# Kernel tuning notes

Hardware: AMD Instinct MI355X
Metric: run time of the kernel (lower is better)

## Reference

```python
import jax, jax.numpy as jnp
import numpy as np

V, E, U = 50257, 256, 256
B, T = 32, 512


def setup_inputs() -> dict:
    key = jax.random.key(0)
    ks = jax.random.split(key, 8)
    s = 0.02  # small init keeps relu-LSTM numerically stable over 512 steps
    return {
        "tokens": jax.random.randint(ks[0], (B, T), 0, V, dtype=jnp.int32),
        "emb": jax.random.normal(ks[1], (V, E), jnp.float32) * s,
        "Wk_f": jax.random.normal(ks[2], (E, 4 * U), jnp.float32) * s,
        "Wr_f": jax.random.normal(ks[3], (U, 4 * U), jnp.float32) * s,
        "b_f": jnp.zeros((4 * U,), jnp.float32),
        "Wk_b": jax.random.normal(ks[4], (E, 4 * U), jnp.float32) * s,
        "Wr_b": jax.random.normal(ks[5], (U, 4 * U), jnp.float32) * s,
        "b_b": jnp.zeros((4 * U,), jnp.float32),
    }


def _lstm_relu(xw, mask, Wr):
    """xw: [T,B,4U] precomputed x@Wk+b; mask: [T,B,1] bool; Wr: [U,4U].
    Keras LSTM with activation='relu', recurrent_activation='sigmoid',
    gate order i,f,g,o. Masked steps carry state & output."""
    u = Wr.shape[0]
    b = xw.shape[1]
    h0 = jnp.zeros((b, u), xw.dtype)
    c0 = jnp.zeros((b, u), xw.dtype)

    def step(carry, inp):
        h, c = carry
        z_x, m = inp
        z = z_x + h @ Wr  # [B,4U]
        i, f, g, o = jnp.split(z, 4, axis=-1)
        i = jax.nn.sigmoid(i)
        f = jax.nn.sigmoid(f)
        g = jax.nn.relu(g)
        o = jax.nn.sigmoid(o)
        c_new = f * c + i * g
        h_new = o * jax.nn.relu(c_new)
        h2 = jnp.where(m, h_new, h)
        c2 = jnp.where(m, c_new, c)
        return (h2, c2), h2

    (hT, cT), ys = jax.lax.scan(step, (h0, c0), (xw, mask))
    return ys, hT, cT  # ys: [T,B,U]


def reference(tokens, emb, Wk_f, Wr_f, b_f, Wk_b, Wr_b, b_b):
    x = emb[tokens]                    # [B,T,E]
    mask = (tokens != 0)[..., None]    # [B,T,1] mask_zero=True
    # forward direction
    xw_f = (x @ Wk_f + b_f).transpose(1, 0, 2)   # [T,B,4U]
    m_f = mask.transpose(1, 0, 2)                # [T,B,1]
    ys_f, hf, cf = _lstm_relu(xw_f, m_f, Wr_f)
    # backward direction: reversed sequence, then re-reverse outputs
    xw_b = (x @ Wk_b + b_b)[:, ::-1].transpose(1, 0, 2)
    m_b = mask[:, ::-1].transpose(1, 0, 2)
    ys_b, hb, cb = _lstm_relu(xw_b, m_b, Wr_b)
    ys_b = ys_b[::-1]
    encoder_outputs = jnp.concatenate([ys_f, ys_b], axis=-1).transpose(1, 0, 2)  # [B,T,2U]
    # NOTE: original module concatenates f_state_h with b_state_c (bug kept faithfully)
    encoder_state_h = jnp.concatenate([hf, cb], axis=-1)  # [B,2U]
    encoder_state_c = jnp.concatenate([cf, cb], axis=-1)  # [B,2U]
    return encoder_outputs, encoder_state_h, encoder_state_c
```

## Files before the change

kernel.cpp:

```cpp
#include <hip/hip_runtime.h>
#include <hip/hip_bf16.h>

#define TT 512
#define BB 32
#define EE 256
#define UU 256
#define NG 1024

typedef unsigned int u32;
typedef unsigned long long u64;
typedef unsigned short u16;
typedef __attribute__((ext_vector_type(8))) short short8;
typedef __attribute__((ext_vector_type(4))) float f32x4;

__device__ __forceinline__ float bf2f(u16 u) { return __uint_as_float(((u32)u) << 16); }
__device__ __forceinline__ u16 f2bf(float f) {
    u32 x = __float_as_uint(f);
    u32 r = (x + 0x7fffu + ((x >> 16) & 1u)) >> 16;
    return (u16)r;
}

__launch_bounds__(256)
__global__ void xw_gemm(const int* __restrict__ tokens,
                        const float* __restrict__ emb,
                        const float* __restrict__ Wk_f, const float* __restrict__ b_f,
                        const float* __restrict__ Wk_b, const float* __restrict__ b_b,
                        u16* __restrict__ xw)
{
    const int dir = blockIdx.z;
    const float* Wk   = dir ? Wk_b : Wk_f;
    const float* bias = dir ? b_b  : b_f;
    const int bn = blockIdx.x;
    const int bm = blockIdx.y;
    const int tid = threadIdx.x;

    __shared__ __align__(16) float At[32][68];
    __shared__ __align__(16) float Bs[32][132];

    float acc[8][4];
#pragma unroll
    for (int i = 0; i < 8; i++)
#pragma unroll
        for (int j = 0; j < 4; j++) acc[i][j] = 0.f;

    const int tx = tid & 31;
    const int ty = tid >> 5;
    const int c0 = tx * 4;
    const int r0 = ty * 8;

    const int lr = tid >> 3;
    const int lk = (tid & 7) * 4;

    for (int k0 = 0; k0 < EE; k0 += 32) {
#pragma unroll
        for (int p = 0; p < 2; p++) {
            int r = lr + p * 32;
            int row = bm * 64 + r;
            int tok = tokens[row];
            const float4 v = *reinterpret_cast<const float4*>(&emb[(size_t)tok * EE + k0 + lk]);
            At[lk + 0][r] = v.x; At[lk + 1][r] = v.y; At[lk + 2][r] = v.z; At[lk + 3][r] = v.w;
        }
        {
            int ck = (tid & 31) * 4;
            int kk = tid >> 5;
#pragma unroll
            for (int p = 0; p < 4; p++) {
                int k = kk + p * 8;
                const float4 v = *reinterpret_cast<const float4*>(&Wk[(size_t)(k0 + k) * NG + bn * 128 + ck]);
                *reinterpret_cast<float4*>(&Bs[k][ck]) = v;
            }
        }
        __syncthreads();
#pragma unroll 8
        for (int k = 0; k < 32; k++) {
            float4 a0 = *reinterpret_cast<const float4*>(&At[k][r0]);
            float4 a1 = *reinterpret_cast<const float4*>(&At[k][r0 + 4]);
            float4 b0 = *reinterpret_cast<const float4*>(&Bs[k][c0]);
            float a[8] = {a0.x, a0.y, a0.z, a0.w, a1.x, a1.y, a1.z, a1.w};
            float b[4] = {b0.x, b0.y, b0.z, b0.w};
#pragma unroll
            for (int i = 0; i < 8; i++)
#pragma unroll
                for (int j = 0; j < 4; j++)
                    acc[i][j] = fmaf(a[i], b[j], acc[i][j]);
        }
        __syncthreads();
    }

    float4 bv = *reinterpret_cast<const float4*>(&bias[bn * 128 + c0]);
    float bias4[4] = {bv.x, bv.y, bv.z, bv.w};
    const int cbase = bn * 128 + c0;
    const int gate  = cbase >> 8;
    const int unitv = cbase & 255;
    const int ugx   = unitv >> 5;
    const int wcol  = gate * 32 + (unitv & 31);
#pragma unroll
    for (int i = 0; i < 8; i++) {
        int row = bm * 64 + r0 + i;
        int b = row >> 9;
        int t = row & 511;
        int t2 = dir ? (TT - 1 - t) : t;
        size_t base = ((((size_t)(dir * TT + t2)) * 8 + ugx) * BB + b) * 128 + wcol;
        ushort4 st;
        st.x = f2bf(acc[i][0] + bias4[0]);
        st.y = f2bf(acc[i][1] + bias4[1]);
        st.z = f2bf(acc[i][2] + bias4[2]);
        st.w = f2bf(acc[i][3] + bias4[3]);
        *reinterpret_cast<ushort4*>(&xw[base]) = st;
    }
}

__device__ __forceinline__ u64 ld_agent(const u64* p) {
    return __hip_atomic_load(p, __ATOMIC_RELAXED, __HIP_MEMORY_SCOPE_AGENT);
}

__launch_bounds__(256, 1)
__global__ void lstm_rec(const int* __restrict__ tokens,
                         const u16* __restrict__ xw,
                         const float* __restrict__ Wr_f,
                         const float* __restrict__ Wr_b,
                         u64* __restrict__ hgq,
                         float* __restrict__ out)
{
    const int wg  = blockIdx.x;
    const int dir = wg >> 3;
    const int ug  = wg & 7;
    const int unit0 = ug * 32;
    const int tid = threadIdx.x;
    const int wv  = tid >> 6;
    const int l   = tid & 63;

    __shared__ __align__(16) u32   HsW[32 * 128];
    __shared__ __align__(16) float Zs[2][BB][132];

    const float* Wr = dir ? Wr_b : Wr_f;
    short8 bfrag[8][2];
    {
        const int col = wv * UU + unit0 + (l & 15);
#pragma unroll
        for (int kt = 0; kt < 8; kt++) {
#pragma unroll
            for (int nt = 0; nt < 2; nt++) {
                int k0 = kt * 32 + (l >> 4) * 8;
                short8 v;
#pragma unroll
                for (int jj = 0; jj < 8; jj++)
                    v[jj] = (short)f2bf(Wr[(size_t)(k0 + jj) * NG + col + nt * 16]);
                bfrag[kt][nt] = v;
            }
        }
    }

    const int cb = tid >> 3;
    const int cj = tid & 7;
    float c_st[4] = {0.f, 0.f, 0.f, 0.f};
    float h_st[4] = {0.f, 0.f, 0.f, 0.f};

    const u16* xwD = xw + (size_t)dir * TT * 8 * BB * 128;
    u64 pxw[4];
    int ptok;
    {
        const u16* p = xwD + (((size_t)0 * 8 + ug) * BB + cb) * 128 + cj * 4;
#pragma unroll
        for (int g = 0; g < 4; g++)
            pxw[g] = *reinterpret_cast<const u64*>(p + g * 32);
        ptok = tokens[cb * TT + (dir ? (TT - 1) : 0)];
    }

    float* outs_h = out + (size_t)BB * TT * 512;
    float* outs_c = outs_h + (size_t)BB * 512;

    for (int s = 0; s < TT; s++) {
        const int p = s & 1;
        f32x4 acc[2][2];
#pragma unroll
        for (int mt = 0; mt < 2; mt++)
#pragma unroll
            for (int nt = 0; nt < 2; nt++) acc[mt][nt] = (f32x4){0.f, 0.f, 0.f, 0.f};

        if (s > 0) {
            const u64* hb = hgq + (size_t)(p * 2 + dir) * 4096 + wv * 1024 + l;
            const u64 tp = (u64)(u32)s | ((u64)(u32)s << 32);
            u64 ql[16];
#pragma unroll
            for (int j = 0; j < 16; j++) ql[j] = ld_agent(hb + j * 64);
            while (true) {
                u64 bad = 0;
#pragma unroll
                for (int j = 0; j < 16; j++) bad |= ql[j] ^ tp;
                if (__all((bad & 0x0000FFFF0000FFFFull) == 0ull)) break;
                __builtin_amdgcn_s_sleep(1);
#pragma unroll
                for (int j = 0; j < 16; j++) ql[j] = ld_agent(hb + j * 64);
            }
#pragma unroll
            for (int j = 0; j < 16; j++) {
                u32 w32 = (((u32)(ql[j] >> 16)) & 0xFFFFu) | (((u32)(ql[j] >> 48)) << 16);
                int ugs = wv * 2 + (j >> 3);
                int b   = (j * 4 + (l >> 4)) & 31;
                int pos = l & 15;
                int g   = ugs * 4 + (pos >> 2);
                HsW[b * 128 + ((g ^ (b & 7)) << 2) + (pos & 3)] = w32;
            }
            __syncthreads();

#pragma unroll
            for (int kt = 0; kt < 8; kt++) {
#pragma unroll
                for (int mt = 0; mt < 2; mt++) {
                    int b = mt * 16 + (l & 15);
                    int g = kt * 4 + (l >> 4);
                    short8 af = *reinterpret_cast<const short8*>(
                        &HsW[b * 128 + ((g ^ (b & 7)) << 2)]);
                    acc[mt][0] = __builtin_amdgcn_mfma_f32_16x16x32_bf16(af, bfrag[kt][0], acc[mt][0], 0, 0, 0);
                    acc[mt][1] = __builtin_amdgcn_mfma_f32_16x16x32_bf16(af, bfrag[kt][1], acc[mt][1], 0, 0, 0);
                }
            }
        }

#pragma unroll
        for (int mt = 0; mt < 2; mt++)
#pragma unroll
            for (int nt = 0; nt < 2; nt++)
#pragma unroll
                for (int r = 0; r < 4; r++)
                    Zs[p][mt * 16 + (l >> 4) * 4 + r][wv * 32 + nt * 16 + (l & 15)] = acc[mt][nt][r];
        __syncthreads();

        float h2[4], c2[4];
        {
            const bool m = (ptok != 0);
#pragma unroll
            for (int q = 0; q < 4; q++) {
                float zi = Zs[p][cb][0 * 32 + cj * 4 + q] + bf2f((u16)(pxw[0] >> (16 * q)));
                float zf = Zs[p][cb][1 * 32 + cj * 4 + q] + bf2f((u16)(pxw[1] >> (16 * q)));
                float zg = Zs[p][cb][2 * 32 + cj * 4 + q] + bf2f((u16)(pxw[2] >> (16 * q)));
                float zo = Zs[p][cb][3 * 32 + cj * 4 + q] + bf2f((u16)(pxw[3] >> (16 * q)));
                float ii = 1.f / (1.f + __expf(-zi));
                float ff = 1.f / (1.f + __expf(-zf));
                float gg = fmaxf(zg, 0.f);
                float oo = 1.f / (1.f + __expf(-zo));
                float cn = ff * c_st[q] + ii * gg;
                float hn = oo * fmaxf(cn, 0.f);
                h2[q] = m ? hn : h_st[q];
                c2[q] = m ? cn : c_st[q];
                h_st[q] = h2[q];
                c_st[q] = c2[q];
            }
        }

        {
            const u32 tagn = (u32)(s + 1);
            u32 t0 = ((u32)f2bf(h2[0]) << 16) | tagn;
            u32 t1 = ((u32)f2bf(h2[1]) << 16) | tagn;
            u32 t2 = ((u32)f2bf(h2[2]) << 16) | tagn;
            u32 t3 = ((u32)f2bf(h2[3]) << 16) | tagn;
            u64 lo = (u64)t0 | ((u64)t1 << 32);
            u64 hi = (u64)t2 | ((u64)t3 << 32);
            u64* hd = hgq + (size_t)(((s + 1) & 1) * 2 + dir) * 4096 + (ug * 32 + cb) * 16 + cj * 2;
            __hip_atomic_store(hd + 0, lo, __ATOMIC_RELAXED, __HIP_MEMORY_SCOPE_AGENT);
            __hip_atomic_store(hd + 1, hi, __ATOMIC_RELAXED, __HIP_MEMORY_SCOPE_AGENT);
        }

        const int tv = dir ? (TT - 1 - s) : s;
        *reinterpret_cast<float4*>(&out[((size_t)cb * TT + tv) * 512 + dir * UU + unit0 + cj * 4]) =
            make_float4(h2[0], h2[1], h2[2], h2[3]);
        if (s == TT - 1) {
            if (dir == 0) {
                *reinterpret_cast<float4*>(&outs_h[cb * 512 + unit0 + cj * 4]) = make_float4(h2[0], h2[1], h2[2], h2[3]);
                *reinterpret_cast<float4*>(&outs_c[cb * 512 + unit0 + cj * 4]) = make_float4(c2[0], c2[1], c2[2], c2[3]);
            } else {
                *reinterpret_cast<float4*>(&outs_h[cb * 512 + UU + unit0 + cj * 4]) = make_float4(c2[0], c2[1], c2[2], c2[3]);
                *reinterpret_cast<float4*>(&outs_c[cb * 512 + UU + unit0 + cj * 4]) = make_float4(c2[0], c2[1], c2[2], c2[3]);
            }
        }
        if (s + 1 < TT) {
            const u16* px = xwD + (((size_t)(s + 1) * 8 + ug) * BB + cb) * 128 + cj * 4;
#pragma unroll
            for (int g = 0; g < 4; g++)
                pxw[g] = *reinterpret_cast<const u64*>(px + g * 32);
            ptok = tokens[cb * TT + (dir ? (TT - 2 - s) : (s + 1))];
        }
    }
}

extern "C" void kernel_launch(void* const* d_in, const int* in_sizes, int n_in,
                              void* d_out, int out_size, void* d_ws, size_t ws_size,
                              hipStream_t stream) {
    const int*   tokens = (const int*)d_in[0];
    const float* emb    = (const float*)d_in[1];
    const float* Wk_f   = (const float*)d_in[2];
    const float* Wr_f   = (const float*)d_in[3];
    const float* b_f    = (const float*)d_in[4];
    const float* Wk_b   = (const float*)d_in[5];
    const float* Wr_b   = (const float*)d_in[6];
    const float* b_b    = (const float*)d_in[7];
    float* out = (float*)d_out;

    char* ws = (char*)d_ws;
    u16* xw  = (u16*)ws;
    u64* hgq = (u64*)(ws + 67108864);

    hipMemsetAsync(hgq, 0, 262144, stream);
    dim3 g1(8, 256, 2);
    xw_gemm<<<g1, 256, 0, stream>>>(tokens, emb, Wk_f, b_f, Wk_b, b_b, xw);
    lstm_rec<<<16, 256, 0, stream>>>(tokens, xw, Wr_f, Wr_b, hgq, out);
}
```

Before: 1.683 ms.

## Co-locate recurrent workgroups on one XCD and poll h-state through L2

Launches 128 workgroups and uses an atomic election on the hardware XCC ID to keep 16 active workgroups on a single XCD (or split across two). The other workgroups exit. Polling of the exchanged hidden state then uses sc0 global loads that are served from that XCD's shared L2, which should cut per-step cross-die synchronisation latency. If polling keeps failing it falls back to agent-scope polling and periodically re-stores its own data. Per-launch epoch-hashed tags replace the memset of the exchange buffer. The change also prefetches the next step's xw earlier and uses nontemporal output stores. It adds risks: 16-bit tags can collide with stale data, the control words live in the tail of the output buffer, and correctness depends on timeouts and restores.

```diff
diff --git a/kernel.cpp b/kernel.cpp
--- a/kernel.cpp
+++ b/kernel.cpp
@@ -12,6 +12,9 @@
 typedef unsigned short u16;
 typedef __attribute__((ext_vector_type(8))) short short8;
 typedef __attribute__((ext_vector_type(4))) float f32x4;
+typedef __attribute__((ext_vector_type(4))) u32 u32x4;
+
+#define TAGMASK 0x0000FFFF0000FFFFull
 
 __device__ __forceinline__ float bf2f(u16 u) { return __uint_as_float(((u32)u) << 16); }
 __device__ __forceinline__ u16 f2bf(float f) {
@@ -114,24 +117,98 @@
     return __hip_atomic_load(p, __ATOMIC_RELAXED, __HIP_MEMORY_SCOPE_AGENT);
 }
 
+__device__ __forceinline__ void poll16_l2(u64 b0, u32 voff, u64* q) {
+    asm volatile(
+        "global_load_dwordx2 %[q0], %[vo], %[b0] sc0\n\t"
+        "global_load_dwordx2 %[q1], %[vo], %[b0] offset:512 sc0\n\t"
+        "global_load_dwordx2 %[q2], %[vo], %[b0] offset:1024 sc0\n\t"
+        "global_load_dwordx2 %[q3], %[vo], %[b0] offset:1536 sc0\n\t"
+        "global_load_dwordx2 %[q4], %[vo], %[b0] offset:2048 sc0\n\t"
+        "global_load_dwordx2 %[q5], %[vo], %[b0] offset:2560 sc0\n\t"
+        "global_load_dwordx2 %[q6], %[vo], %[b0] offset:3072 sc0\n\t"
+        "global_load_dwordx2 %[q7], %[vo], %[b0] offset:3584 sc0\n\t"
+        "global_load_dwordx2 %[q8], %[vo], %[b1] sc0\n\t"
+        "global_load_dwordx2 %[q9], %[vo], %[b1] offset:512 sc0\n\t"
+        "global_load_dwordx2 %[q10], %[vo], %[b1] offset:1024 sc0\n\t"
+        "global_load_dwordx2 %[q11], %[vo], %[b1] offset:1536 sc0\n\t"
+        "global_load_dwordx2 %[q12], %[vo], %[b1] offset:2048 sc0\n\t"
+        "global_load_dwordx2 %[q13], %[vo], %[b1] offset:2560 sc0\n\t"
+        "global_load_dwordx2 %[q14], %[vo], %[b1] offset:3072 sc0\n\t"
+        "global_load_dwordx2 %[q15], %[vo], %[b1] offset:3584 sc0\n\t"
+        "s_waitcnt vmcnt(0)"
+        : [q0]"=&v"(q[0]), [q1]"=&v"(q[1]), [q2]"=&v"(q[2]), [q3]"=&v"(q[3]),
+          [q4]"=&v"(q[4]), [q5]"=&v"(q[5]), [q6]"=&v"(q[6]), [q7]"=&v"(q[7]),
+          [q8]"=&v"(q[8]), [q9]"=&v"(q[9]), [q10]"=&v"(q[10]), [q11]"=&v"(q[11]),
+          [q12]"=&v"(q[12]), [q13]"=&v"(q[13]), [q14]"=&v"(q[14]), [q15]"=&v"(q[15])
+        : [vo]"v"(voff), [b0]"s"(b0), [b1]"s"(b0 + 4096ull)
+        : "memory");
+}
+
+__device__ __forceinline__ void dual_store(u64* hd, u64 lo, u64 hi) {
+    u32x4 v = (u32x4){(u32)lo, (u32)(lo >> 32), (u32)hi, (u32)(hi >> 32)};
+    asm volatile("global_store_dwordx4 %[a], %[d], off sc0"
+                 :: [a]"v"(hd), [d]"v"(v) : "memory");
+    __hip_atomic_store(hd + 0, lo, __ATOMIC_RELAXED, __HIP_MEMORY_SCOPE_AGENT);
+    __hip_atomic_store(hd + 1, hi, __ATOMIC_RELAXED, __HIP_MEMORY_SCOPE_AGENT);
+}
+
 __launch_bounds__(256, 1)
 __global__ void lstm_rec(const int* __restrict__ tokens,
                          const u16* __restrict__ xw,
                          const float* __restrict__ Wr_f,
                          const float* __restrict__ Wr_b,
                          u64* __restrict__ hgq,
+                         int* __restrict__ ctl,
                          float* __restrict__ out)
 {
-    const int wg  = blockIdx.x;
-    const int dir = wg >> 3;
-    const int ug  = wg & 7;
+    const int tid = threadIdx.x;
+
+    __shared__ int s_role, s_epoch;
+    __shared__ __align__(16) u32   HsW[32 * 128];
+    __shared__ __align__(16) float Zs[2][BB][132];
+
+    if (tid == 0) {
+        u32 xcc;
+        asm volatile("s_getreg_b32 %0, hwreg(HW_REG_XCC_ID)" : "=s"(xcc));
+        xcc &= 7u;
+        u32* cnt = (u32*)(ctl + 4);
+        u32 slot = atomicAdd(&cnt[xcc], 1u);
+        if (slot == 7u) {
+            if (atomicCAS(&ctl[0], -1, (int)xcc) == -1) {
+                u64 rt = __builtin_amdgcn_s_memrealtime();
+                int ep = (int)((((u32)rt ^ (u32)(rt >> 32)) & 0x7FFFFFFEu) | 1u);
+                atomicExch(&ctl[2], ep);
+            } else {
+                atomicCAS(&ctl[1], -1, (int)xcc);
+            }
+        } else if (slot == 15u) {
+            atomicCAS(&ctl[1], -1, (int)xcc);
+        }
+        int w0, w1, ep;
+        for (;;) {
+            w0 = __hip_atomic_load(&ctl[0], __ATOMIC_RELAXED, __HIP_MEMORY_SCOPE_AGENT);
+            w1 = __hip_atomic_load(&ctl[1], __ATOMIC_RELAXED, __HIP_MEMORY_SCOPE_AGENT);
+            ep = __hip_atomic_load(&ctl[2], __ATOMIC_RELAXED, __HIP_MEMORY_SCOPE_AGENT);
+            if (w0 >= 0 && w1 >= 0 && ep != -1) break;
+            __builtin_amdgcn_s_sleep(8);
+        }
+        int role = -1;
+        if ((int)xcc == w0 && slot < 8u) role = (int)slot;
+        else if (w1 == w0 && (int)xcc == w0 && slot >= 8u && slot < 16u) role = (int)slot;
+        else if (w1 != w0 && (int)xcc == w1 && slot < 8u) role = 8 + (int)slot;
+        s_role = role;
+        s_epoch = ep;
+    }
+    __syncthreads();
+    const int role = s_role;
+    const u32 tagbase = (u32)s_epoch * 2654435761u;
+    if (role < 0) return;
+
+    const int dir = role >> 3;
+    const int ug  = role & 7;
     const int unit0 = ug * 32;
-    const int tid = threadIdx.x;
     const int wv  = tid >> 6;
     const int l   = tid & 63;
-
-    __shared__ __align__(16) u32   HsW[32 * 128];
-    __shared__ __align__(16) float Zs[2][BB][132];
 
     const float* Wr = dir ? Wr_b : Wr_f;
     short8 bfrag[8][2];
@@ -155,6 +232,18 @@
     const int cj = tid & 7;
     float c_st[4] = {0.f, 0.f, 0.f, 0.f};
     float h_st[4] = {0.f, 0.f, 0.f, 0.f};
+
+    u64* const hdP[2] = {
+        hgq + (size_t)(0 * 2 + dir) * 4096 + (ug * 32 + cb) * 16 + cj * 2,
+        hgq + (size_t)(1 * 2 + dir) * 4096 + (ug * 32 + cb) * 16 + cj * 2
+    };
+    u64 myLo[2] = {0ull, 0ull}, myHi[2] = {0ull, 0ull};
+
+    auto restoreMine = [&](int s_) {
+        const int cpar = s_ & 1;
+        dual_store(hdP[cpar], myLo[cpar], myHi[cpar]);
+        if (s_ >= 2) dual_store(hdP[cpar ^ 1], myLo[cpar ^ 1], myHi[cpar ^ 1]);
+    };
 
     const u16* xwD = xw + (size_t)dir * TT * 8 * BB * 128;
     u64 pxw[4];
@@ -170,6 +259,9 @@
     float* outs_h = out + (size_t)BB * TT * 512;
     float* outs_c = outs_h + (size_t)BB * 512;
 
+    bool sc0mode = true;
+    int  sc0fail = 0;
+
     for (int s = 0; s < TT; s++) {
         const int p = s & 1;
         f32x4 acc[2][2];
@@ -178,21 +270,56 @@
 #pragma unroll
             for (int nt = 0; nt < 2; nt++) acc[mt][nt] = (f32x4){0.f, 0.f, 0.f, 0.f};
 
+        u64 ql[16];
         if (s > 0) {
+            const u32 tg = (tagbase + (u32)s) & 0xFFFFu;
+            const u64 tp = (u64)tg | ((u64)tg << 32);
             const u64* hb = hgq + (size_t)(p * 2 + dir) * 4096 + wv * 1024 + l;
-            const u64 tp = (u64)(u32)s | ((u64)(u32)s << 32);
-            u64 ql[16];
-#pragma unroll
-            for (int j = 0; j < 16; j++) ql[j] = ld_agent(hb + j * 64);
-            while (true) {
-                u64 bad = 0;
-#pragma unroll
-                for (int j = 0; j < 16; j++) bad |= ql[j] ^ tp;
-                if (__all((bad & 0x0000FFFF0000FFFFull) == 0ull)) break;
-                __builtin_amdgcn_s_sleep(1);
-#pragma unroll
-                for (int j = 0; j < 16; j++) ql[j] = ld_agent(hb + j * 64);
-            }
+            bool ok = false;
+            if (sc0mode) {
+                u64 hb_u = (u64)(hgq + (size_t)(p * 2 + dir) * 4096 + wv * 1024);
+                u32 blo = __builtin_amdgcn_readfirstlane((u32)hb_u);
+                u32 bhi = __builtin_amdgcn_readfirstlane((u32)(hb_u >> 32));
+                u64 hbs = ((u64)bhi << 32) | blo;
+                const u32 vo = (u32)(l << 3);
+                for (int r = 0; r < 12; ++r) {
+                    poll16_l2(hbs, vo, ql);
+                    u64 bad = 0;
+#pragma unroll
+                    for (int j = 0; j < 16; j++) bad |= ql[j] ^ tp;
+                    if (__all((bad & TAGMASK) == 0ull)) { ok = true; break; }
+                    __builtin_amdgcn_s_sleep(1);
+                    if (r == 5) restoreMine(s);
+                }
+            }
+            if (!ok) {
+                if (sc0mode && ++sc0fail >= 3) sc0mode = false;
+                int rr = 0;
+                for (;;) {
+#pragma unroll
+                    for (int j = 0; j < 16; j++) ql[j] = ld_agent(hb + j * 64);
+                    u64 bad = 0;
+#pragma unroll
+                    for (int j = 0; j < 16; j++) bad |= ql[j] ^ tp;
+                    if (__all((bad & TAGMASK) == 0ull)) break;
+                    __builtin_amdgcn_s_sleep(1);
+                    if (((++rr) & 7) == 0) restoreMine(s);
+                }
+            } else {
+                sc0fail = 0;
+            }
+        }
+
+        u64 pxw2[4]; int ptok2 = 0;
+        if (s + 1 < TT) {
+            const u16* px = xwD + (((size_t)(s + 1) * 8 + ug) * BB + cb) * 128 + cj * 4;
+#pragma unroll
+            for (int g = 0; g < 4; g++)
+                pxw2[g] = __builtin_nontemporal_load(reinterpret_cast<const u64*>(px + g * 32));
+            ptok2 = tokens[cb * TT + (dir ? (TT - 2 - s) : (s + 1))];
+        }
+
+        if (s > 0) {
 #pragma unroll
             for (int j = 0; j < 16; j++) {
                 u32 w32 = (((u32)(ql[j] >> 16)) & 0xFFFFu) | (((u32)(ql[j] >> 48)) << 16);
@@ -250,36 +377,37 @@
         }
 
         {
-            const u32 tagn = (u32)(s + 1);
+            const u32 tagn = (tagbase + (u32)(s + 1)) & 0xFFFFu;
             u32 t0 = ((u32)f2bf(h2[0]) << 16) | tagn;
             u32 t1 = ((u32)f2bf(h2[1]) << 16) | tagn;
             u32 t2 = ((u32)f2bf(h2[2]) << 16) | tagn;
             u32 t3 = ((u32)f2bf(h2[3]) << 16) | tagn;
             u64 lo = (u64)t0 | ((u64)t1 << 32);
             u64 hi = (u64)t2 | ((u64)t3 << 32);
-            u64* hd = hgq + (size_t)(((s + 1) & 1) * 2 + dir) * 4096 + (ug * 32 + cb) * 16 + cj * 2;
-            __hip_atomic_store(hd + 0, lo, __ATOMIC_RELAXED, __HIP_MEMORY_SCOPE_AGENT);
-            __hip_atomic_store(hd + 1, hi, __ATOMIC_RELAXED, __HIP_MEMORY_SCOPE_AGENT);
+            const int par = (s + 1) & 1;
+            dual_store(hdP[par], lo, hi);
+            myLo[par] = lo; myHi[par] = hi;
         }
 
         const int tv = dir ? (TT - 1 - s) : s;
-        *reinterpret_cast<float4*>(&out[((size_t)cb * TT + tv) * 512 + dir * UU + unit0 + cj * 4]) =
-            make_float4(h2[0], h2[1], h2[2], h2[3]);
+        {
+            f32x4 ov = (f32x4){h2[0], h2[1], h2[2], h2[3]};
+            __builtin_nontemporal_store(ov,
+                reinterpret_cast<f32x4*>(&out[((size_t)cb * TT + tv) * 512 + dir * UU + unit0 + cj * 4]));
+        }
         if (s == TT - 1) {
             if (dir == 0) {
-                *reinterpret_cast<float4*>(&outs_h[cb * 512 + unit0 + cj * 4]) = make_float4(h2[0], h2[1], h2[2], h2[3]);
-                *reinterpret_cast<float4*>(&outs_c[cb * 512 + unit0 + cj * 4]) = make_float4(c2[0], c2[1], c2[2], c2[3]);
+                *reinterpret_cast<f32x4*>(&outs_h[cb * 512 + unit0 + cj * 4]) = (f32x4){h2[0], h2[1], h2[2], h2[3]};
+                *reinterpret_cast<f32x4*>(&outs_c[cb * 512 + unit0 + cj * 4]) = (f32x4){c2[0], c2[1], c2[2], c2[3]};
             } else {
-                *reinterpret_cast<float4*>(&outs_h[cb * 512 + UU + unit0 + cj * 4]) = make_float4(c2[0], c2[1], c2[2], c2[3]);
-                *reinterpret_cast<float4*>(&outs_c[cb * 512 + UU + unit0 + cj * 4]) = make_float4(c2[0], c2[1], c2[2], c2[3]);
+                *reinterpret_cast<f32x4*>(&outs_h[cb * 512 + UU + unit0 + cj * 4]) = (f32x4){c2[0], c2[1], c2[2], c2[3]};
+                *reinterpret_cast<f32x4*>(&outs_c[cb * 512 + UU + unit0 + cj * 4]) = (f32x4){c2[0], c2[1], c2[2], c2[3]};
             }
         }
         if (s + 1 < TT) {
-            const u16* px = xwD + (((size_t)(s + 1) * 8 + ug) * BB + cb) * 128 + cj * 4;
-#pragma unroll
-            for (int g = 0; g < 4; g++)
-                pxw[g] = *reinterpret_cast<const u64*>(px + g * 32);
-            ptok = tokens[cb * TT + (dir ? (TT - 2 - s) : (s + 1))];
+#pragma unroll
+            for (int g = 0; g < 4; g++) pxw[g] = pxw2[g];
+            ptok = ptok2;
         }
     }
 }
@@ -301,8 +429,11 @@
     u16* xw  = (u16*)ws;
     u64* hgq = (u64*)(ws + 67108864);
 
-    hipMemsetAsync(hgq, 0, 262144, stream);
+    char* ctl = (char*)d_out + (size_t)out_size - 64;
+
+    (void)hipMemsetAsync(ctl, 0xFF, 12, stream);
+    (void)hipMemsetAsync(ctl + 16, 0, 32, stream);
     dim3 g1(8, 256, 2);
     xw_gemm<<<g1, 256, 0, stream>>>(tokens, emb, Wk_f, b_f, Wk_b, b_b, xw);
-    lstm_rec<<<16, 256, 0, stream>>>(tokens, xw, Wr_f, Wr_b, hgq, out);
-}
+    lstm_rec<<<128, 256, 0, stream>>>(tokens, xw, Wr_f, Wr_b, hgq, (int*)ctl, out);
+}
```

After: 3.336 ms. 1.98x slower.

## Fuse input GEMM into recurrent kernel with per-timestep readiness flags

Applied to the files above, without the earlier changes.

Merges the embedding/input-projection GEMM and the LSTM recurrence into one launch. Blocks 0-15 run the recurrence, and the remaining blocks compute xw tiles in time-major order, then raise per-timestep counters. Recurrent blocks spin on these flags before loading each step's xw, so the GEMM overlaps the serial recurrence instead of running before it. The cost is spin-waiting, atomic loads and stores, and the assumption that the 16 recurrent blocks become resident together with the GEMM blocks, or the launch can deadlock.

```diff
diff --git a/kernel.cpp b/kernel.cpp
--- a/kernel.cpp
+++ b/kernel.cpp
@@ -20,118 +20,125 @@
     return (u16)r;
 }
 
-__launch_bounds__(256)
-__global__ void xw_gemm(const int* __restrict__ tokens,
-                        const float* __restrict__ emb,
-                        const float* __restrict__ Wk_f, const float* __restrict__ b_f,
-                        const float* __restrict__ Wk_b, const float* __restrict__ b_b,
-                        u16* __restrict__ xw)
-{
-    const int dir = blockIdx.z;
-    const float* Wk   = dir ? Wk_b : Wk_f;
-    const float* bias = dir ? b_b  : b_f;
-    const int bn = blockIdx.x;
-    const int bm = blockIdx.y;
-    const int tid = threadIdx.x;
-
-    __shared__ __align__(16) float At[32][68];
-    __shared__ __align__(16) float Bs[32][132];
-
-    float acc[8][4];
-#pragma unroll
-    for (int i = 0; i < 8; i++)
-#pragma unroll
-        for (int j = 0; j < 4; j++) acc[i][j] = 0.f;
-
-    const int tx = tid & 31;
-    const int ty = tid >> 5;
-    const int c0 = tx * 4;
-    const int r0 = ty * 8;
-
-    const int lr = tid >> 3;
-    const int lk = (tid & 7) * 4;
-
-    for (int k0 = 0; k0 < EE; k0 += 32) {
-#pragma unroll
-        for (int p = 0; p < 2; p++) {
-            int r = lr + p * 32;
-            int row = bm * 64 + r;
-            int tok = tokens[row];
-            const float4 v = *reinterpret_cast<const float4*>(&emb[(size_t)tok * EE + k0 + lk]);
-            At[lk + 0][r] = v.x; At[lk + 1][r] = v.y; At[lk + 2][r] = v.z; At[lk + 3][r] = v.w;
-        }
-        {
-            int ck = (tid & 31) * 4;
-            int kk = tid >> 5;
-#pragma unroll
-            for (int p = 0; p < 4; p++) {
-                int k = kk + p * 8;
-                const float4 v = *reinterpret_cast<const float4*>(&Wk[(size_t)(k0 + k) * NG + bn * 128 + ck]);
-                *reinterpret_cast<float4*>(&Bs[k][ck]) = v;
-            }
-        }
-        __syncthreads();
-#pragma unroll 8
-        for (int k = 0; k < 32; k++) {
-            float4 a0 = *reinterpret_cast<const float4*>(&At[k][r0]);
-            float4 a1 = *reinterpret_cast<const float4*>(&At[k][r0 + 4]);
-            float4 b0 = *reinterpret_cast<const float4*>(&Bs[k][c0]);
-            float a[8] = {a0.x, a0.y, a0.z, a0.w, a1.x, a1.y, a1.z, a1.w};
-            float b[4] = {b0.x, b0.y, b0.z, b0.w};
-#pragma unroll
-            for (int i = 0; i < 8; i++)
-#pragma unroll
-                for (int j = 0; j < 4; j++)
-                    acc[i][j] = fmaf(a[i], b[j], acc[i][j]);
-        }
-        __syncthreads();
-    }
-
-    float4 bv = *reinterpret_cast<const float4*>(&bias[bn * 128 + c0]);
-    float bias4[4] = {bv.x, bv.y, bv.z, bv.w};
-    const int cbase = bn * 128 + c0;
-    const int gate  = cbase >> 8;
-    const int unitv = cbase & 255;
-    const int ugx   = unitv >> 5;
-    const int wcol  = gate * 32 + (unitv & 31);
-#pragma unroll
-    for (int i = 0; i < 8; i++) {
-        int row = bm * 64 + r0 + i;
-        int b = row >> 9;
-        int t = row & 511;
-        int t2 = dir ? (TT - 1 - t) : t;
-        size_t base = ((((size_t)(dir * TT + t2)) * 8 + ugx) * BB + b) * 128 + wcol;
-        ushort4 st;
-        st.x = f2bf(acc[i][0] + bias4[0]);
-        st.y = f2bf(acc[i][1] + bias4[1]);
-        st.z = f2bf(acc[i][2] + bias4[2]);
-        st.w = f2bf(acc[i][3] + bias4[3]);
-        *reinterpret_cast<ushort4*>(&xw[base]) = st;
-    }
-}
-
 __device__ __forceinline__ u64 ld_agent(const u64* p) {
     return __hip_atomic_load(p, __ATOMIC_RELAXED, __HIP_MEMORY_SCOPE_AGENT);
 }
 
 __launch_bounds__(256, 1)
-__global__ void lstm_rec(const int* __restrict__ tokens,
-                         const u16* __restrict__ xw,
-                         const float* __restrict__ Wr_f,
-                         const float* __restrict__ Wr_b,
-                         u64* __restrict__ hgq,
-                         float* __restrict__ out)
+__global__ void fused(const int* __restrict__ tokens,
+                      const float* __restrict__ emb,
+                      const float* __restrict__ Wk_f, const float* __restrict__ b_f,
+                      const float* __restrict__ Wk_b, const float* __restrict__ b_b,
+                      const float* __restrict__ Wr_f, const float* __restrict__ Wr_b,
+                      u16* __restrict__ xw,
+                      u64* __restrict__ hgq,
+                      u32* __restrict__ tflag,
+                      float* __restrict__ out)
 {
+    const int tid = threadIdx.x;
+    __shared__ __align__(16) char smem[50688];
+
+    if (blockIdx.x >= 16) {
+        const int gid = blockIdx.x - 16;
+        const int dirg = gid & 1;
+        const int g2   = gid >> 1;
+        const int bn   = g2 & 7;
+        const int bmT  = g2 >> 3;
+        const float* Wk   = dirg ? Wk_b : Wk_f;
+        const float* bias = dirg ? b_b  : b_f;
+
+        float (*At)[68]  = reinterpret_cast<float(*)[68]>(smem);
+        float (*Bs)[132] = reinterpret_cast<float(*)[132]>(smem + 8704);
+
+        float acc[8][4];
+#pragma unroll
+        for (int i = 0; i < 8; i++)
+#pragma unroll
+            for (int j = 0; j < 4; j++) acc[i][j] = 0.f;
+
+        const int tx = tid & 31;
+        const int ty = tid >> 5;
+        const int c0 = tx * 4;
+        const int r0 = ty * 8;
+        const int lr = tid >> 3;
+        const int lk = (tid & 7) * 4;
+
+        for (int k0 = 0; k0 < EE; k0 += 32) {
+#pragma unroll
+            for (int p = 0; p < 2; p++) {
+                int r  = lr + p * 32;
+                int rp = bmT * 64 + r;
+                int t2 = rp >> 5, b = rp & 31;
+                int t  = dirg ? (TT - 1 - t2) : t2;
+                int tok = tokens[b * TT + t];
+                const float4 v = *reinterpret_cast<const float4*>(&emb[(size_t)tok * EE + k0 + lk]);
+                At[lk + 0][r] = v.x; At[lk + 1][r] = v.y; At[lk + 2][r] = v.z; At[lk + 3][r] = v.w;
+            }
+            {
+                int ck = (tid & 31) * 4;
+                int kk = tid >> 5;
+#pragma unroll
+                for (int p = 0; p < 4; p++) {
+                    int k = kk + p * 8;
+                    const float4 v = *reinterpret_cast<const float4*>(&Wk[(size_t)(k0 + k) * NG + bn * 128 + ck]);
+                    *reinterpret_cast<float4*>(&Bs[k][ck]) = v;
+                }
+            }
+            __syncthreads();
+#pragma unroll 8
+            for (int k = 0; k < 32; k++) {
+                float4 a0 = *reinterpret_cast<const float4*>(&At[k][r0]);
+                float4 a1 = *reinterpret_cast<const float4*>(&At[k][r0 + 4]);
+                float4 b0 = *reinterpret_cast<const float4*>(&Bs[k][c0]);
+                float a[8] = {a0.x, a0.y, a0.z, a0.w, a1.x, a1.y, a1.z, a1.w};
+                float b[4] = {b0.x, b0.y, b0.z, b0.w};
+#pragma unroll
+                for (int i = 0; i < 8; i++)
+#pragma unroll
+                    for (int j = 0; j < 4; j++)
+                        acc[i][j] = fmaf(a[i], b[j], acc[i][j]);
+            }
+            __syncthreads();
+        }
+
+        float4 bv = *reinterpret_cast<const float4*>(&bias[bn * 128 + c0]);
+        float bias4[4] = {bv.x, bv.y, bv.z, bv.w};
+        const int cbase = bn * 128 + c0;
+        const int gate  = cbase >> 8;
+        const int unitv = cbase & 255;
+        const int ugx   = unitv >> 5;
+        const int wcol  = gate * 32 + (unitv & 31);
+#pragma unroll
+        for (int i = 0; i < 8; i++) {
+            int r  = r0 + i;
+            int rp = bmT * 64 + r;
+            int t2 = rp >> 5, b = rp & 31;
+            size_t base = ((((size_t)(dirg * TT + t2)) * 8 + ugx) * BB + b) * 128 + wcol;
+            u64 pk = (u64)f2bf(acc[i][0] + bias4[0])
+                   | ((u64)f2bf(acc[i][1] + bias4[1]) << 16)
+                   | ((u64)f2bf(acc[i][2] + bias4[2]) << 32)
+                   | ((u64)f2bf(acc[i][3] + bias4[3]) << 48);
+            __hip_atomic_store(reinterpret_cast<u64*>(&xw[base]), pk,
+                               __ATOMIC_RELAXED, __HIP_MEMORY_SCOPE_AGENT);
+        }
+        __threadfence();
+        __syncthreads();
+        if (tid < 2) {
+            __hip_atomic_fetch_add(&tflag[dirg * TT + bmT * 2 + tid], 1u,
+                                   __ATOMIC_RELAXED, __HIP_MEMORY_SCOPE_AGENT);
+        }
+        return;
+    }
+
     const int wg  = blockIdx.x;
     const int dir = wg >> 3;
     const int ug  = wg & 7;
     const int unit0 = ug * 32;
-    const int tid = threadIdx.x;
     const int wv  = tid >> 6;
     const int l   = tid & 63;
 
-    __shared__ __align__(16) u32   HsW[32 * 128];
-    __shared__ __align__(16) float Zs[2][BB][132];
+    u32*  HsW = reinterpret_cast<u32*>(smem);
+    float (*Zs)[BB][132] = reinterpret_cast<float(*)[BB][132]>(smem + 16384);
 
     const float* Wr = dir ? Wr_b : Wr_f;
     short8 bfrag[8][2];
@@ -156,14 +163,21 @@
     float c_st[4] = {0.f, 0.f, 0.f, 0.f};
     float h_st[4] = {0.f, 0.f, 0.f, 0.f};
 
+    const u32* myflag = tflag + dir * TT;
+    auto waitFlag = [&](int t2) {
+        while (__hip_atomic_load(&myflag[t2], __ATOMIC_RELAXED, __HIP_MEMORY_SCOPE_AGENT) < 8u)
+            __builtin_amdgcn_s_sleep(8);
+    };
+
     const u16* xwD = xw + (size_t)dir * TT * 8 * BB * 128;
     u64 pxw[4];
     int ptok;
     {
+        waitFlag(0);
         const u16* p = xwD + (((size_t)0 * 8 + ug) * BB + cb) * 128 + cj * 4;
 #pragma unroll
         for (int g = 0; g < 4; g++)
-            pxw[g] = *reinterpret_cast<const u64*>(p + g * 32);
+            pxw[g] = ld_agent(reinterpret_cast<const u64*>(p + g * 32));
         ptok = tokens[cb * TT + (dir ? (TT - 1) : 0)];
     }
 
@@ -275,10 +289,11 @@
             }
         }
         if (s + 1 < TT) {
+            waitFlag(s + 1);
             const u16* px = xwD + (((size_t)(s + 1) * 8 + ug) * BB + cb) * 128 + cj * 4;
 #pragma unroll
             for (int g = 0; g < 4; g++)
-                pxw[g] = *reinterpret_cast<const u64*>(px + g * 32);
+                pxw[g] = ld_agent(reinterpret_cast<const u64*>(px + g * 32));
             ptok = tokens[cb * TT + (dir ? (TT - 2 - s) : (s + 1))];
         }
     }
@@ -298,11 +313,11 @@
     float* out = (float*)d_out;
 
     char* ws = (char*)d_ws;
-    u16* xw  = (u16*)ws;
-    u64* hgq = (u64*)(ws + 67108864);
-
-    hipMemsetAsync(hgq, 0, 262144, stream);
-    dim3 g1(8, 256, 2);
-    xw_gemm<<<g1, 256, 0, stream>>>(tokens, emb, Wk_f, b_f, Wk_b, b_b, xw);
-    lstm_rec<<<16, 256, 0, stream>>>(tokens, xw, Wr_f, Wr_b, hgq, out);
+    u16* xw    = (u16*)ws;
+    u64* hgq   = (u64*)(ws + 67108864);
+    u32* tflag = (u32*)(ws + 67108864 + 131072);
+
+    (void)hipMemsetAsync(ws + 67108864, 0, 135168, stream);
+    fused<<<4112, 256, 0, stream>>>(tokens, emb, Wk_f, b_f, Wk_b, b_b,
+                                    Wr_f, Wr_b, xw, hgq, tflag, out);
 }
```

After: 1.969 ms. 17.0% more time.
